# Kernel tuning notes

Hardware: AMD Instinct MI355X
Metric: run time of the kernel (lower is better)

Reference implementation:

```python
import jax, jax.numpy as jnp
import numpy as np

D_MODEL = 1024
N_HEADS = 16
D_KEY = 64
EPS = 1e-5


def setup_inputs() -> dict:
    key = jax.random.key(0)
    ks = jax.random.split(key, 12)
    d, h, dk = D_MODEL, N_HEADS, D_KEY
    s = lambda fan_in: 1.0 / np.sqrt(fan_in)
    inp = {
        "X": jax.random.normal(ks[0], (2, 2048, d), dtype=jnp.float32),
        "Wqkv": jax.random.uniform(ks[1], (d, 3 * h * dk), jnp.float32, -s(d), s(d)),
        "bqkv": jax.random.uniform(ks[2], (3 * h * dk,), jnp.float32, -s(d), s(d)),
        "Wo": jax.random.uniform(ks[3], (h * dk, d), jnp.float32, -s(h * dk), s(h * dk)),
        "bo": jax.random.uniform(ks[4], (d,), jnp.float32, -s(h * dk), s(h * dk)),
        "W1": jax.random.uniform(ks[5], (d, 4 * d), jnp.float32, -s(d), s(d)),
        "b1": jax.random.uniform(ks[6], (4 * d,), jnp.float32, -s(d), s(d)),
        "W2": jax.random.uniform(ks[7], (4 * d, d), jnp.float32, -s(4 * d), s(4 * d)),
        "b2": jax.random.uniform(ks[8], (d,), jnp.float32, -s(4 * d), s(4 * d)),
        "ln1_g": jnp.ones((d,), jnp.float32),
        "ln1_b": jnp.zeros((d,), jnp.float32),
        "ln2_g": jnp.ones((d,), jnp.float32),
        "ln2_b": jnp.zeros((d,), jnp.float32),
    }
    return inp


def _layernorm(x, g, b):
    mu = jnp.mean(x, axis=-1, keepdims=True)
    var = jnp.var(x, axis=-1, keepdims=True)
    return (x - mu) * jax.lax.rsqrt(var + EPS) * g + b


def _block(X, Wqkv, bqkv, Wo, bo, W1, b1, W2, b2, ln1_g, ln1_b, ln2_g, ln2_b):
    B, T, _ = X.shape
    h, dk = N_HEADS, D_KEY
    # --- causal multi-head self-attention on LN(X) ---
    Xn = _layernorm(X, ln1_g, ln1_b)
    qkv = (Xn @ Wqkv + bqkv).reshape(B, T, 3, h, dk)
    q, k, v = (jnp.moveaxis(qkv, 2, 0)[i].transpose(0, 2, 1, 3) for i in range(3))  # each [B,h,T,dk]
    scores = jnp.einsum("bhqd,bhkd->bhqk", q, k) / np.sqrt(dk).astype(np.float32)
    causal = jnp.tril(jnp.ones((T, T), dtype=bool))
    scores = jnp.where(causal, scores, -jnp.inf)
    attn = jax.nn.softmax(scores, axis=-1)
    ctx = jnp.einsum("bhqk,bhkd->bhqd", attn, v)  # [B,h,T,dk]
    ctx = ctx.transpose(0, 2, 1, 3).reshape(B, T, h * dk)
    atten = ctx @ Wo + bo
    X = X + atten  # dropout is identity in eval mode
    # --- FFN on LN(X) ---
    Xn2 = _layernorm(X, ln2_g, ln2_b)
    ffn = jax.nn.relu(Xn2 @ W1 + b1) @ W2 + b2
    return X + ffn


def reference(X, Wqkv, bqkv, Wo, bo, W1, b1, W2, b2, ln1_g, ln1_b, ln2_g, ln2_b):
    return _block(X, Wqkv, bqkv, Wo, bo, W1, b1, W2, b2, ln1_g, ln1_b, ln2_g, ln2_b)
```

## Files before the change

### kernel.cpp

```cpp
#include <hip/hip_runtime.h>
#include <hip/hip_bf16.h>

typedef __hip_bfloat16 bf16;
typedef __attribute__((ext_vector_type(8))) short short8;
typedef __attribute__((ext_vector_type(4))) float f32x4;

constexpr int D     = 1024;
constexpr int T     = 2048;
constexpr int BATCH = 2;
constexpr int ROWS  = BATCH * T;
constexpr int NH    = 16;
constexpr int DKEY  = 64;
constexpr int QKVN  = 3 * D;
constexpr int FFNN  = 4 * D;

static __device__ __forceinline__ float b2f(bf16 x) { return __bfloat162float(x); }
static __device__ __forceinline__ bf16  f2b(float x) { return __float2bfloat16(x); }
static __device__ __forceinline__ float loadf(const bf16* p)  { return __bfloat162float(*p); }
static __device__ __forceinline__ float loadf(const float* p) { return *p; }
static __device__ __forceinline__ float fast_exp2(float x) { return __builtin_amdgcn_exp2f(x); }
static __device__ __forceinline__ unsigned short f2bu(float x) {
    return __bfloat16_as_ushort(__float2bfloat16(x));
}

__global__ __launch_bounds__(256) void transpose_cast(const float* __restrict__ in,
                                                      bf16* __restrict__ out,
                                                      int R, int C)
{
    __shared__ float tile[32][33];
    int c0 = blockIdx.x * 32, r0 = blockIdx.y * 32;
    int tx = threadIdx.x & 31, ty = threadIdx.x >> 5;
#pragma unroll
    for (int i = 0; i < 32; i += 8)
        tile[ty + i][tx] = in[(size_t)(r0 + ty + i) * C + c0 + tx];
    __syncthreads();
#pragma unroll
    for (int i = 0; i < 32; i += 8)
        out[(size_t)(c0 + ty + i) * R + r0 + tx] = f2b(tile[tx][ty + i]);
}

template <typename TIN>
__global__ __launch_bounds__(256) void ln_kernel(const TIN* __restrict__ X,
                                                 const float* __restrict__ g,
                                                 const float* __restrict__ b,
                                                 bf16* __restrict__ out)
{
    int row = blockIdx.x;
    int tid = threadIdx.x;
    const TIN* xr = X + (size_t)row * D;
    float v[4];
#pragma unroll
    for (int i = 0; i < 4; ++i) v[i] = loadf(xr + tid + i * 256);

    float s1 = v[0] + v[1] + v[2] + v[3];
    float s2 = v[0]*v[0] + v[1]*v[1] + v[2]*v[2] + v[3]*v[3];
#pragma unroll
    for (int off = 32; off; off >>= 1) {
        s1 += __shfl_xor(s1, off);
        s2 += __shfl_xor(s2, off);
    }
    __shared__ float red[8];
    int lane = tid & 63, w = tid >> 6;
    if (lane == 0) { red[w] = s1; red[4 + w] = s2; }
    __syncthreads();
    s1 = red[0] + red[1] + red[2] + red[3];
    s2 = red[4] + red[5] + red[6] + red[7];

    float mu   = s1 * (1.0f / D);
    float var  = s2 * (1.0f / D) - mu * mu;
    float rstd = rsqrtf(var + 1e-5f);

    bf16* orow = out + (size_t)row * D;
#pragma unroll
    for (int i = 0; i < 4; ++i) {
        int c = tid + i * 256;
        orow[c] = f2b((v[i] - mu) * rstd * g[c] + b[c]);
    }
}

template <int BM, int RELU, int RES, int OUTF32, int SPLITZ = 0>
__global__ __launch_bounds__(256) void mfma_gemm(
    const bf16* __restrict__ A, const bf16* __restrict__ Bt,
    const float* __restrict__ bias, const void* __restrict__ resid,
    void* __restrict__ out, float* __restrict__ part,
    int M, int N, int K, int Kstride)
{
    constexpr int LDSK = 40;
    constexpr int MT   = BM / 32;
    __shared__ __align__(16) unsigned short As[2][BM * LDSK];
    __shared__ __align__(16) unsigned short Bs[2][128 * LDSK];

    int gx = gridDim.x, gy = gridDim.y;
    int lid = (blockIdx.z * gy + blockIdx.y) * gx + blockIdx.x;
    int nwg = gx * gy * gridDim.z;
    int chunk = nwg >> 3;
    int swz = (lid & 7) * chunk + (lid >> 3);
    int bx = swz % gx;
    int by = (swz / gx) % gy;
    int bz = swz / (gx * gy);

    int tid  = threadIdx.x;
    int m0   = by * BM, n0 = bx * 128;
    int lane = tid & 63, wave = tid >> 6;
    int wm = (wave >> 1) * (MT * 16), wn = (wave & 1) * 64;
    int c15 = lane & 15, quad = lane >> 4;

    int koff = 0;
    if constexpr (SPLITZ) koff = bz * K;

    f32x4 acc[MT][4] = {};

    int brow = tid >> 1, bseg = (tid & 1) * 16;
    int arow, aseg;
    if constexpr (BM == 128) { arow = tid >> 1; aseg = (tid & 1) * 16; }
    else                     { arow = tid >> 2; aseg = (tid & 3) * 8;  }
    const bf16* aptr = A  + (size_t)(m0 + arow) * Kstride + koff + aseg;
    const bf16* bptr = Bt + (size_t)(n0 + brow) * Kstride + koff + bseg;

    int nk = K >> 5;
    uint4 ra0, ra1, rb0, rb1;
    ra0 = *(const uint4*)(aptr);
    if constexpr (BM == 128) ra1 = *(const uint4*)(aptr + 8);
    rb0 = *(const uint4*)(bptr);
    rb1 = *(const uint4*)(bptr + 8);

    for (int kt = 0; kt < nk; ++kt) {
        int buf = kt & 1;
        {
            unsigned short* asl = &As[buf][arow * LDSK + aseg];
            unsigned short* bsl = &Bs[buf][brow * LDSK + bseg];
            *(uint4*)asl = ra0;
            if constexpr (BM == 128) *(uint4*)(asl + 8) = ra1;
            *(uint4*)bsl       = rb0;
            *(uint4*)(bsl + 8) = rb1;
        }
        __syncthreads();
        if (kt + 1 < nk) {
            int ko = (kt + 1) * 32;
            ra0 = *(const uint4*)(aptr + ko);
            if constexpr (BM == 128) ra1 = *(const uint4*)(aptr + ko + 8);
            rb0 = *(const uint4*)(bptr + ko);
            rb1 = *(const uint4*)(bptr + ko + 8);
        }
        short8 af[MT], bfr[4];
#pragma unroll
        for (int t = 0; t < MT; ++t)
            af[t]  = *(const short8*)&As[buf][(wm + t * 16 + c15) * LDSK + quad * 8];
#pragma unroll
        for (int t = 0; t < 4; ++t)
            bfr[t] = *(const short8*)&Bs[buf][(wn + t * 16 + c15) * LDSK + quad * 8];
#pragma unroll
        for (int mt = 0; mt < MT; ++mt)
#pragma unroll
            for (int nt = 0; nt < 4; ++nt)
                acc[mt][nt] = __builtin_amdgcn_mfma_f32_16x16x32_bf16(
                    af[mt], bfr[nt], acc[mt][nt], 0, 0, 0);
    }

#pragma unroll
    for (int mt = 0; mt < MT; ++mt) {
#pragma unroll
        for (int nt = 0; nt < 4; ++nt) {
            f32x4 v4 = acc[mt][nt];
            int gc = n0 + wn + nt * 16 + c15;
            float bb = (!SPLITZ || bz == 0) ? bias[gc] : 0.0f;
#pragma unroll
            for (int r = 0; r < 4; ++r) {
                int gr = m0 + wm + mt * 16 + quad * 4 + r;
                float v = v4[r] + bb;
                if constexpr (RELU) v = fmaxf(v, 0.0f);
                size_t idx = (size_t)gr * N + gc;
                if constexpr (SPLITZ) {
                    if (bz == 0) {
                        v += b2f(((const bf16*)resid)[idx]);
                        ((float*)out)[idx] = v;
                    } else {
                        part[idx] = v;
                    }
                } else {
                    if constexpr (RES == 1) v += b2f(((const bf16*)resid)[idx]);
                    if constexpr (RES == 2) v += ((const float*)resid)[idx];
                    if constexpr (OUTF32) ((float*)out)[idx] = v;
                    else                  ((bf16*)out)[idx] = f2b(v);
                }
            }
        }
    }
}

__global__ __launch_bounds__(256) void add_partial(float* __restrict__ out,
                                                   const float* __restrict__ part)
{
    int i = blockIdx.x * 256 + threadIdx.x;
    f32x4 a = ((const f32x4*)out)[i];
    f32x4 p = ((const f32x4*)part)[i];
    a += p;
    ((f32x4*)out)[i] = a;
}

__global__ __launch_bounds__(256) void flash_attn(const bf16* __restrict__ qkv,
                                                  bf16* __restrict__ ctx)
{
    constexpr int KROW = 72;
    constexpr float CSC = 0.18033688011112042f;
    constexpr float MSH = 12.0f;

    __shared__ __align__(16) unsigned short Qs[128 * KROW];
    __shared__ __align__(16) unsigned short Ks[64 * KROW];
    __shared__ __align__(16) unsigned short Vt[64 * KROW];
    unsigned short* Pt = Qs;

    int bx = blockIdx.x;
    int bh = bx & 31;
    int qi = 15 - (bx >> 5);
    int h  = bh & 15, b = bh >> 4;
    int q0 = qi * 128;

    int tid = threadIdx.x, lane = tid & 63, w = tid >> 6;
    int c15 = lane & 15, quad = lane >> 4;

    const bf16* base = qkv + (size_t)b * T * QKVN;

    {
        int row = tid >> 1, half = tid & 1;
        const bf16* src = base + (size_t)(q0 + row) * QKVN + h * 64 + half * 32;
        unsigned short* dst = &Qs[row * KROW + half * 32];
        uint4 v0 = *(const uint4*)(src);
        uint4 v1 = *(const uint4*)(src + 8);
        uint4 v2 = *(const uint4*)(src + 16);
        uint4 v3 = *(const uint4*)(src + 24);
        *(uint4*)(dst)      = v0;
        *(uint4*)(dst + 8)  = v1;
        *(uint4*)(dst + 16) = v2;
        *(uint4*)(dst + 24) = v3;
    }
    __syncthreads();

    short8 qf[2][2];
#pragma unroll
    for (int qt = 0; qt < 2; ++qt)
#pragma unroll
        for (int s = 0; s < 2; ++s)
            qf[qt][s] = *(const short8*)&Qs[(w * 32 + qt * 16 + c15) * KROW + s * 32 + quad * 8];

    short8 ones;
#pragma unroll
    for (int i = 0; i < 8; ++i) ones[i] = (short)0x3F80;

    f32x4 Ot[4][2] = {};
    f32x4 lacc[2]  = {};

    int nkt   = q0 / 64 + 2;
    int wqmin = q0 + w * 32;
    int wqmax = wqmin + 31;

    for (int kt = 0; kt < nkt; ++kt) {
        int k0 = kt * 64;
        int key = tid >> 2, seg = tid & 3;
        const bf16* ksrc = base + (size_t)(k0 + key) * QKVN + D + h * 64 + seg * 16;
        uint4 kv0 = *(const uint4*)ksrc;
        uint4 kv1 = *(const uint4*)(ksrc + 8);
        int keyp = (tid & 31) * 2, dk0 = (tid >> 5) * 8;
        const bf16* vsrc = base + (size_t)(k0 + keyp) * QKVN + 2 * D + h * 64 + dk0;
        uint4 vv0 = *(const uint4*)vsrc;
        uint4 vv1 = *(const uint4*)(vsrc + QKVN);

        __syncthreads();
        {
            unsigned short* kd = &Ks[key * KROW + seg * 16];
            *(uint4*)kd       = kv0;
            *(uint4*)(kd + 8) = kv1;
            const unsigned short* lo = (const unsigned short*)&vv0;
            const unsigned short* hi = (const unsigned short*)&vv1;
#pragma unroll
            for (int j = 0; j < 8; ++j) {
                unsigned int pk = (unsigned int)lo[j] | ((unsigned int)hi[j] << 16);
                *(unsigned int*)&Vt[(dk0 + j) * KROW + keyp] = pk;
            }
        }
        __syncthreads();

        if (k0 <= wqmax) {
            f32x4 St[4][2] = {};
#pragma unroll
            for (int s = 0; s < 2; ++s)
#pragma unroll
                for (int ktm = 0; ktm < 4; ++ktm) {
                    short8 kf = *(const short8*)&Ks[(ktm * 16 + c15) * KROW + s * 32 + quad * 8];
#pragma unroll
                    for (int qt = 0; qt < 2; ++qt)
                        St[ktm][qt] = __builtin_amdgcn_mfma_f32_16x16x32_bf16(
                            kf, qf[qt][s], St[ktm][qt], 0, 0, 0);
                }

            bool diag = (k0 + 63 > wqmin);
#pragma unroll
            for (int ktm = 0; ktm < 4; ++ktm)
#pragma unroll
                for (int qt = 0; qt < 2; ++qt) {
                    ushort4 pk;
                    int q_g = wqmin + qt * 16 + c15;
#pragma unroll
                    for (int r = 0; r < 4; ++r) {
                        float p = fast_exp2(fmaf(St[ktm][qt][r], CSC, -MSH));
                        if (diag && (k0 + ktm * 16 + quad * 4 + r > q_g)) p = 0.0f;
                        ((unsigned short*)&pk)[r] = f2bu(p);
                    }
                    *(ushort4*)&Pt[(w * 32 + qt * 16 + c15) * KROW + ktm * 16 + quad * 4] = pk;
                }

#pragma unroll
            for (int s = 0; s < 2; ++s) {
                short8 pf[2];
#pragma unroll
                for (int qt = 0; qt < 2; ++qt)
                    pf[qt] = *(const short8*)&Pt[(w * 32 + qt * 16 + c15) * KROW + s * 32 + quad * 8];
#pragma unroll
                for (int qt = 0; qt < 2; ++qt)
                    lacc[qt] = __builtin_amdgcn_mfma_f32_16x16x32_bf16(ones, pf[qt], lacc[qt], 0, 0, 0);
#pragma unroll
                for (int dt = 0; dt < 4; ++dt) {
                    short8 vf = *(const short8*)&Vt[(dt * 16 + c15) * KROW + s * 32 + quad * 8];
#pragma unroll
                    for (int qt = 0; qt < 2; ++qt)
                        Ot[dt][qt] = __builtin_amdgcn_mfma_f32_16x16x32_bf16(
                            vf, pf[qt], Ot[dt][qt], 0, 0, 0);
                }
            }
        }
    }

#pragma unroll
    for (int qt = 0; qt < 2; ++qt) {
        float inv = 1.0f / lacc[qt][0];
        int grow = b * T + q0 + w * 32 + qt * 16 + c15;
        bf16* dst = ctx + (size_t)grow * D + h * 64 + quad * 4;
#pragma unroll
        for (int dt = 0; dt < 4; ++dt) {
            ushort4 pk;
#pragma unroll
            for (int r = 0; r < 4; ++r)
                ((unsigned short*)&pk)[r] = f2bu(Ot[dt][qt][r] * inv);
            *(ushort4*)(dst + dt * 16) = pk;
        }
    }
}

extern "C" void kernel_launch(void* const* d_in, const int* in_sizes, int n_in,
                              void* d_out, int out_size, void* d_ws, size_t ws_size,
                              hipStream_t stream)
{
    const float* X    = (const float*)d_in[0];
    const float* Wqkv = (const float*)d_in[1];
    const float* bqkv = (const float*)d_in[2];
    const float* Wo   = (const float*)d_in[3];
    const float* bo   = (const float*)d_in[4];
    const float* W1   = (const float*)d_in[5];
    const float* b1   = (const float*)d_in[6];
    const float* W2   = (const float*)d_in[7];
    const float* b2   = (const float*)d_in[8];
    const float* ln1g = (const float*)d_in[9];
    const float* ln1b = (const float*)d_in[10];
    const float* ln2g = (const float*)d_in[11];
    const float* ln2b = (const float*)d_in[12];
    float* out = (float*)d_out;

    char* ws = (char*)d_ws;
    bf16* Wqkv_t = (bf16*)(ws + 0);
    bf16* Wo_t   = (bf16*)(ws + 6291456);
    bf16* W1_t   = (bf16*)(ws + 8388608);
    bf16* W2_t   = (bf16*)(ws + 16777216);
    bf16* Xn     = (bf16*)(ws + 25165824);
    bf16* X1     = Xn;
    bf16* qkv    = (bf16*)(ws + 33554432);
    bf16* Xn2    = (bf16*)(ws + 33554432);
    bf16* ctx    = (bf16*)(ws + 58720256);
    bf16* mid    = (bf16*)(ws + 41943040);
    float* W2part = (float*)(ws + 0);

    transpose_cast<<<dim3(QKVN / 32, D / 32), 256, 0, stream>>>(Wqkv, Wqkv_t, D, QKVN);
    transpose_cast<<<dim3(D / 32, D / 32), 256, 0, stream>>>(Wo, Wo_t, D, D);
    transpose_cast<<<dim3(FFNN / 32, D / 32), 256, 0, stream>>>(W1, W1_t, D, FFNN);
    transpose_cast<<<dim3(D / 32, FFNN / 32), 256, 0, stream>>>(W2, W2_t, FFNN, D);

    ln_kernel<float><<<ROWS, 256, 0, stream>>>(X, ln1g, ln1b, Xn);
    mfma_gemm<128, 0, 0, 0><<<dim3(QKVN / 128, ROWS / 128), 256, 0, stream>>>(
        Xn, Wqkv_t, bqkv, nullptr, qkv, nullptr, ROWS, QKVN, D, D);
    flash_attn<<<512, 256, 0, stream>>>(qkv, ctx);
    mfma_gemm<64, 0, 2, 0><<<dim3(D / 128, ROWS / 64), 256, 0, stream>>>(
        ctx, Wo_t, bo, X, X1, nullptr, ROWS, D, D, D);
    ln_kernel<bf16><<<ROWS, 256, 0, stream>>>(X1, ln2g, ln2b, Xn2);
    mfma_gemm<128, 1, 0, 0><<<dim3(FFNN / 128, ROWS / 128), 256, 0, stream>>>(
        Xn2, W1_t, b1, nullptr, mid, nullptr, ROWS, FFNN, D, D);
    mfma_gemm<64, 0, 1, 1, 1><<<dim3(D / 128, ROWS / 64, 2), 256, 0, stream>>>(
        mid, W2_t, b2, X1, out, W2part, ROWS, D, FFNN / 2, FFNN);
    add_partial<<<ROWS * D / 4 / 256, 256, 0, stream>>>(out, W2part);
}
```

Measured before the change: 372.0 us.

## Stage GEMM tiles via direct global-to-LDS loads with double buffering

Replaces the register-staged global loads and LDS stores in the MFMA GEMM with global_load_lds DMA-style loads that write straight into shared memory. The next tile is issued into the alternate buffer before the current tile is computed, with one barrier per iteration. This removes the VGPR round trip and the separate LDS writes. In exchange the LDS rows lose their padding (stride 32 instead of 40), which may cause bank conflicts on the fragment reads.

```diff
diff --git a/kernel.cpp b/kernel.cpp
--- a/kernel.cpp
+++ b/kernel.cpp
@@ -23,6 +23,13 @@
     return __bfloat16_as_ushort(__float2bfloat16(x));
 }
 
+static __device__ __forceinline__ void gload_lds16(const bf16* g, unsigned short* l) {
+    __builtin_amdgcn_global_load_lds(
+        (const __attribute__((address_space(1))) void*)g,
+        (__attribute__((address_space(3))) void*)l,
+        16, 0, 0);
+}
+
 __global__ __launch_bounds__(256) void transpose_cast(const float* __restrict__ in,
                                                       bf16* __restrict__ out,
                                                       int R, int C)
@@ -85,10 +92,9 @@
     void* __restrict__ out, float* __restrict__ part,
     int M, int N, int K, int Kstride)
 {
-    constexpr int LDSK = 40;
-    constexpr int MT   = BM / 32;
-    __shared__ __align__(16) unsigned short As[2][BM * LDSK];
-    __shared__ __align__(16) unsigned short Bs[2][128 * LDSK];
+    constexpr int MT = BM / 32;
+    __shared__ __align__(16) unsigned short As[2][BM * 32];
+    __shared__ __align__(16) unsigned short Bs[2][128 * 32];
 
     int gx = gridDim.x, gy = gridDim.y;
     int lid = (blockIdx.z * gy + blockIdx.y) * gx + blockIdx.x;
@@ -110,51 +116,56 @@
 
     f32x4 acc[MT][4] = {};
 
-    int brow = tid >> 1, bseg = (tid & 1) * 16;
-    int arow, aseg;
-    if constexpr (BM == 128) { arow = tid >> 1; aseg = (tid & 1) * 16; }
-    else                     { arow = tid >> 2; aseg = (tid & 3) * 8;  }
-    const bf16* aptr = A  + (size_t)(m0 + arow) * Kstride + koff + aseg;
-    const bf16* bptr = Bt + (size_t)(n0 + brow) * Kstride + koff + bseg;
+    int srow = lane >> 2;
+    int scol = (lane & 3) * 8;
+    const bf16* abase = A  + (size_t)m0 * Kstride + koff;
+    const bf16* bbase = Bt + (size_t)n0 * Kstride + koff;
+
+    auto stage = [&](int buf, int kt) {
+        int ko = kt * 32;
+#pragma unroll
+        for (int j = 0; j < 2; ++j) {
+            int r = wave * 32 + j * 16;
+            gload_lds16(bbase + (size_t)(r + srow) * Kstride + ko + scol,
+                        &Bs[buf][r * 32]);
+        }
+        if constexpr (BM == 128) {
+#pragma unroll
+            for (int j = 0; j < 2; ++j) {
+                int r = wave * 32 + j * 16;
+                gload_lds16(abase + (size_t)(r + srow) * Kstride + ko + scol,
+                            &As[buf][r * 32]);
+            }
+        } else {
+            int r = wave * 16;
+            gload_lds16(abase + (size_t)(r + srow) * Kstride + ko + scol,
+                        &As[buf][r * 32]);
+        }
+    };
 
     int nk = K >> 5;
-    uint4 ra0, ra1, rb0, rb1;
-    ra0 = *(const uint4*)(aptr);
-    if constexpr (BM == 128) ra1 = *(const uint4*)(aptr + 8);
-    rb0 = *(const uint4*)(bptr);
-    rb1 = *(const uint4*)(bptr + 8);
+    stage(0, 0);
+    __syncthreads();
 
     for (int kt = 0; kt < nk; ++kt) {
         int buf = kt & 1;
-        {
-            unsigned short* asl = &As[buf][arow * LDSK + aseg];
-            unsigned short* bsl = &Bs[buf][brow * LDSK + bseg];
-            *(uint4*)asl = ra0;
-            if constexpr (BM == 128) *(uint4*)(asl + 8) = ra1;
-            *(uint4*)bsl       = rb0;
-            *(uint4*)(bsl + 8) = rb1;
-        }
-        __syncthreads();
-        if (kt + 1 < nk) {
-            int ko = (kt + 1) * 32;
-            ra0 = *(const uint4*)(aptr + ko);
-            if constexpr (BM == 128) ra1 = *(const uint4*)(aptr + ko + 8);
-            rb0 = *(const uint4*)(bptr + ko);
-            rb1 = *(const uint4*)(bptr + ko + 8);
-        }
+        if (kt + 1 < nk) stage(buf ^ 1, kt + 1);
+
         short8 af[MT], bfr[4];
 #pragma unroll
         for (int t = 0; t < MT; ++t)
-            af[t]  = *(const short8*)&As[buf][(wm + t * 16 + c15) * LDSK + quad * 8];
+            af[t]  = *(const short8*)&As[buf][(wm + t * 16 + c15) * 32 + quad * 8];
 #pragma unroll
         for (int t = 0; t < 4; ++t)
-            bfr[t] = *(const short8*)&Bs[buf][(wn + t * 16 + c15) * LDSK + quad * 8];
+            bfr[t] = *(const short8*)&Bs[buf][(wn + t * 16 + c15) * 32 + quad * 8];
 #pragma unroll
         for (int mt = 0; mt < MT; ++mt)
 #pragma unroll
             for (int nt = 0; nt < 4; ++nt)
                 acc[mt][nt] = __builtin_amdgcn_mfma_f32_16x16x32_bf16(
                     af[mt], bfr[nt], acc[mt][nt], 0, 0, 0);
+
+        __syncthreads();
     }
 
 #pragma unroll
```

New measurement: 362.7 us. 2.5% less time.
